# Performance work log

Measured on AMD Instinct MI355X. Metric: run time of the kernel, lower is better.

## Reference

```python
import jax, jax.numpy as jnp
import numpy as np

DECAY = 0.99


def setup_inputs() -> dict:
    key = jax.random.key(0)
    k1, k2, k3, k4 = jax.random.split(key, 4)
    N, D, K = 65536, 256, 1024
    return {
        "masked_z_e_x": jax.random.normal(k1, (N, D), dtype=jnp.float32),
        "z_e_x": jax.random.normal(k2, (N, D), dtype=jnp.float32),
        "embedding": jax.random.normal(k3, (K, D), dtype=jnp.float32) * (1.0 / K),
        "ema_count": jnp.ones((K,), dtype=jnp.float32),
        "ema_w": jax.random.normal(k4, (K, D), dtype=jnp.float32) * (1.0 / K),
    }


def _vq_indices(x_flat, codebook):
    # distances[n,k] = ||x_n||^2 + ||c_k||^2 - 2 x_n . c_k  (addmm in torch)
    c_sqr = jnp.sum(codebook * codebook, axis=1)              # [K]
    x_sqr = jnp.sum(x_flat * x_flat, axis=1, keepdims=True)   # [N,1]
    dists = x_sqr + c_sqr - 2.0 * (x_flat @ codebook.T)       # [N,K]
    return jnp.argmin(dists, axis=1)                          # [N]


def reference(masked_z_e_x, z_e_x, embedding, ema_count, ema_w):
    K, D = embedding.shape
    x_flat = masked_z_e_x.reshape(-1, D)
    indices = _vq_indices(x_flat, embedding)                  # [N] int

    # straight-through quantized codes (value = gathered codes)
    z_q_x = embedding[indices].reshape(masked_z_e_x.shape)

    # EMA codebook update (training branch); one-hot matmul == segment sums
    z_flat = z_e_x.reshape(-1, D)
    counts = jax.ops.segment_sum(jnp.ones_like(indices, dtype=jnp.float32),
                                 indices, num_segments=K)     # [K]
    dw = jax.ops.segment_sum(z_flat, indices, num_segments=K) # [K,D]
    ema_count_new = DECAY * ema_count + (1.0 - DECAY) * counts
    ema_w_new = DECAY * ema_w + (1.0 - DECAY) * dw
    embedding_new = ema_w_new / ema_count_new[:, None]

    # re-gather from the updated (detached) codebook
    z_q_x_bar = embedding_new[indices].reshape(z_e_x.shape)
    return (z_q_x, z_q_x_bar, embedding_new, ema_count_new, ema_w_new)
```

## Files before the change

kernel.cpp:

```cpp
#include <hip/hip_runtime.h>

#define DDIM 256
#define KCODES 1024
#define MARGIN 2.0e-4f

typedef __attribute__((ext_vector_type(8))) short fragA;
typedef __attribute__((ext_vector_type(4))) float f32x4;

static __device__ __forceinline__ float4 ld4(const float* p) {
    return *reinterpret_cast<const float4*>(p);
}

static __device__ __forceinline__ ushort bf16_rne(float f) {
    unsigned bits = __float_as_uint(f);
    unsigned r = bits + 0x7FFFu + ((bits >> 16) & 1u);
    return (ushort)(r >> 16);
}

__global__ void split_sqnorm_kernel(const float* __restrict__ X, ushort* __restrict__ Xs,
                                    float* __restrict__ out, int nrows) {
    int row = blockIdx.x * 4 + (threadIdx.x >> 6);
    if (row >= nrows) return;
    int lane = threadIdx.x & 63;
    float4 v = reinterpret_cast<const float4*>(X + (size_t)row * DDIM)[lane];
    double s = (double)v.x * v.x + (double)v.y * v.y + (double)v.z * v.z + (double)v.w * v.w;
    #pragma unroll
    for (int off = 32; off > 0; off >>= 1) s += __shfl_down(s, off);
    if (lane == 0) out[row] = (float)s;

    float fv[4] = {v.x, v.y, v.z, v.w};
    ushort hb[4], lb[4];
    #pragma unroll
    for (int i = 0; i < 4; i++) {
        hb[i] = bf16_rne(fv[i]);
        float hf = __uint_as_float((unsigned)hb[i] << 16);
        lb[i] = bf16_rne(fv[i] - hf);
    }
    ushort4 hi = make_ushort4(hb[0], hb[1], hb[2], hb[3]);
    ushort4 lo = make_ushort4(lb[0], lb[1], lb[2], lb[3]);
    *reinterpret_cast<ushort4*>(Xs + (size_t)row * 512 + lane * 4) = hi;
    *reinterpret_cast<ushort4*>(Xs + (size_t)row * 512 + 256 + lane * 4) = lo;
}

__global__ __launch_bounds__(256) void argmin_mfma_kernel(
        const float* __restrict__ X, const ushort* __restrict__ Cs,
        float* __restrict__ xsq, const float* __restrict__ csq,
        int* __restrict__ indices, int* __restrict__ flag_cnt,
        int* __restrict__ flag_list, int nrows_total) {
    __shared__ ushort clds[32 * 512];

    int tid = threadIdx.x;
    int w = tid >> 6;
    int l = tid & 63;
    int lm = l & 15;
    int lg = l >> 4;
    int row0 = blockIdx.x * 64;

    const float* xrowf = X + (size_t)(row0 + w * 16 + lm) * DDIM;
    fragA a_hi[8], a_lo[8];
    double dsum = 0.0;
    #pragma unroll
    for (int s = 0; s < 8; s++) {
        float4 v0 = ld4(xrowf + s * 32 + lg * 8);
        float4 v1 = ld4(xrowf + s * 32 + lg * 8 + 4);
        float f[8] = {v0.x, v0.y, v0.z, v0.w, v1.x, v1.y, v1.z, v1.w};
        fragA h, lo;
        #pragma unroll
        for (int j = 0; j < 8; j++) {
            dsum += (double)f[j] * f[j];
            ushort hb = bf16_rne(f[j]);
            float hf = __uint_as_float((unsigned)hb << 16);
            ushort lb = bf16_rne(f[j] - hf);
            h[j] = (short)hb;
            lo[j] = (short)lb;
        }
        a_hi[s] = h;
        a_lo[s] = lo;
    }
    dsum += __shfl_xor(dsum, 16);
    dsum += __shfl_xor(dsum, 32);
    float xsqf = (float)dsum;
    if (l < 16) xsq[row0 + w * 16 + l] = xsqf;
    float xs_r[4];
    #pragma unroll
    for (int r = 0; r < 4; r++) xs_r[r] = __shfl(xsqf, lg * 4 + r);

    float d1[4], d2[4];
    int k1[4];
    #pragma unroll
    for (int r = 0; r < 4; r++) { d1[r] = 3.0e38f; d2[r] = 3.0e38f; k1[r] = 0; }

    for (int kc = 0; kc < KCODES; kc += 32) {
        __syncthreads();
        #pragma unroll
        for (int it = 0; it < 8; it++) {
            int c = it * 256 + tid;
            int r = c >> 6, col = c & 63;
            int p = (col & 32) | ((col & 31) ^ (r & 7));
            *reinterpret_cast<float4*>(&clds[r * 512 + p * 8]) =
                *reinterpret_cast<const float4*>(Cs + (size_t)(kc + r) * 512 + col * 8);
        }
        __syncthreads();

        f32x4 acc[2];
        #pragma unroll
        for (int kt = 0; kt < 2; kt++) acc[kt] = (f32x4){0.f, 0.f, 0.f, 0.f};

        #pragma unroll
        for (int s = 0; s < 8; s++) {
            #pragma unroll
            for (int kt = 0; kt < 2; kt++) {
                int kl = kt * 16 + lm;
                int chi = (4 * s + lg) ^ (kl & 7);
                fragA bhi = *reinterpret_cast<const fragA*>(&clds[kl * 512 + chi * 8]);
                fragA blo = *reinterpret_cast<const fragA*>(&clds[kl * 512 + (32 + chi) * 8]);
                acc[kt] = __builtin_amdgcn_mfma_f32_16x16x32_bf16(a_hi[s], bhi, acc[kt], 0, 0, 0);
                acc[kt] = __builtin_amdgcn_mfma_f32_16x16x32_bf16(a_lo[s], bhi, acc[kt], 0, 0, 0);
                acc[kt] = __builtin_amdgcn_mfma_f32_16x16x32_bf16(a_hi[s], blo, acc[kt], 0, 0, 0);
            }
        }

        #pragma unroll
        for (int kt = 0; kt < 2; kt++) {
            int k = kc + kt * 16 + lm;
            float cs = csq[k];
            #pragma unroll
            for (int r = 0; r < 4; r++) {
                float dist = (xs_r[r] + cs) - 2.0f * acc[kt][r];
                if (dist < d1[r] || (dist == d1[r] && k < k1[r])) {
                    d2[r] = d1[r]; d1[r] = dist; k1[r] = k;
                } else if (dist < d2[r]) {
                    d2[r] = dist;
                }
            }
        }
    }

    #pragma unroll
    for (int r = 0; r < 4; r++) {
        float bd1 = d1[r], bd2 = d2[r];
        int bk1 = k1[r];
        #pragma unroll
        for (int m = 1; m < 16; m <<= 1) {
            float od1 = __shfl_xor(bd1, m);
            int ok1 = __shfl_xor(bk1, m);
            float od2 = __shfl_xor(bd2, m);
            if (od1 < bd1 || (od1 == bd1 && ok1 < bk1)) {
                bd2 = fminf(bd1, od2); bd1 = od1; bk1 = ok1;
            } else {
                bd2 = fminf(bd2, od1);
            }
        }
        if (lm == 0) {
            int row = row0 + w * 16 + lg * 4 + r;
            indices[row] = bk1;
            if (bd2 - bd1 < MARGIN) {
                int pos = atomicAdd(flag_cnt, 1);
                if (pos < nrows_total) flag_list[pos] = row;
            }
        }
    }
}

#define ECH 64
#define NKCH (KCODES / ECH)

__global__ __launch_bounds__(256) void exact_chunk_kernel(
        const float* __restrict__ X, const float* __restrict__ C,
        const float* __restrict__ xsq, const float* __restrict__ csq,
        const int* __restrict__ flag_cnt, const int* __restrict__ flag_list,
        unsigned long long* __restrict__ best64, int nrows_total) {
    __shared__ float xt[64][36];
    __shared__ float ct[64][36];
    __shared__ int rowidx[64];
    __shared__ float xsql[64];

    int cnt = *flag_cnt;
    if (cnt > nrows_total) cnt = nrows_total;
    if (cnt <= 0) return;
    int ntiles = (cnt + 63) >> 6;
    int nunits = ntiles * NKCH;

    int tid = threadIdx.x;
    int tx = tid & 15;
    int ty = tid >> 4;

    for (int u = blockIdx.x; u < nunits; u += gridDim.x) {
        int t = u >> 4;
        int kc = (u & 15) * ECH;
        int base = t * 64;

        __syncthreads();
        if (tid < 64) {
            int p = base + tid;
            int row = flag_list[p < cnt ? p : base];
            rowidx[tid] = row;
            xsql[tid] = xsq[row];
        }
        __syncthreads();

        float xs[4];
        #pragma unroll
        for (int i = 0; i < 4; i++) xs[i] = xsql[i * 16 + ty];

        float acc[4][4];
        #pragma unroll
        for (int i = 0; i < 4; i++)
            #pragma unroll
            for (int j = 0; j < 4; j++) acc[i][j] = 0.0f;

        for (int dt = 0; dt < DDIM; dt += 32) {
            __syncthreads();
            #pragma unroll
            for (int it = 0; it < 2; it++) {
                int e = it * 256 + tid;
                int r = e >> 3, c4 = e & 7;
                *reinterpret_cast<float4*>(&xt[r][c4 * 4]) =
                    ld4(X + (size_t)rowidx[r] * DDIM + dt + c4 * 4);
            }
            #pragma unroll
            for (int it = 0; it < 2; it++) {
                int e = it * 256 + tid;
                int r = e >> 3, c4 = e & 7;
                *reinterpret_cast<float4*>(&ct[r][c4 * 4]) =
                    ld4(C + (size_t)(kc + r) * DDIM + dt + c4 * 4);
            }
            __syncthreads();

            for (int d4 = 0; d4 < 32; d4 += 4) {
                float4 xv[4], cv[4];
                #pragma unroll
                for (int i = 0; i < 4; i++)
                    xv[i] = *reinterpret_cast<const float4*>(&xt[i * 16 + ty][d4]);
                #pragma unroll
                for (int j = 0; j < 4; j++)
                    cv[j] = *reinterpret_cast<const float4*>(&ct[j * 16 + tx][d4]);
                #pragma unroll
                for (int i = 0; i < 4; i++)
                    #pragma unroll
                    for (int j = 0; j < 4; j++) {
                        float a = acc[i][j];
                        a += xv[i].x * cv[j].x; a += xv[i].y * cv[j].y;
                        a += xv[i].z * cv[j].z; a += xv[i].w * cv[j].w;
                        acc[i][j] = a;
                    }
            }
        }

        float cs_r[4];
        #pragma unroll
        for (int j = 0; j < 4; j++) cs_r[j] = csq[kc + j * 16 + tx];

        #pragma unroll
        for (int i = 0; i < 4; i++) {
            float bd = 3.0e38f; int bk = 0;
            #pragma unroll
            for (int j = 0; j < 4; j++) {
                int kk = kc + j * 16 + tx;
                float tt = xs[i] + cs_r[j];
                float dist = tt - 2.0f * acc[i][j];
                if (dist < bd || (dist == bd && kk < bk)) { bd = dist; bk = kk; }
            }
            #pragma unroll
            for (int m = 1; m < 16; m <<= 1) {
                float od = __shfl_xor(bd, m);
                int ok = __shfl_xor(bk, m);
                if (od < bd || (od == bd && ok < bk)) { bd = od; bk = ok; }
            }
            if (tx == 0) {
                int p = base + i * 16 + ty;
                if (p < cnt) {
                    unsigned long long pk =
                        ((unsigned long long)__float_as_uint(bd) << 32) | (unsigned)bk;
                    atomicMin(&best64[p], pk);
                }
            }
        }
    }
}

__global__ void exact_finalize_kernel(const int* __restrict__ flag_cnt,
                                      const int* __restrict__ flag_list,
                                      const unsigned long long* __restrict__ best64,
                                      int* __restrict__ indices, int nrows_total) {
    int cnt = *flag_cnt;
    if (cnt > nrows_total) cnt = nrows_total;
    for (int i = blockIdx.x * 256 + threadIdx.x; i < cnt; i += gridDim.x * 256)
        indices[flag_list[i]] = (int)(best64[i] & 0xFFFFFFFFULL);
}

__global__ void hist_kernel(const int* __restrict__ idx, int* __restrict__ counts) {
    int i = blockIdx.x * 256 + threadIdx.x;
    atomicAdd(&counts[idx[i]], 1);
}

__global__ void prefix_kernel(const int* __restrict__ counts, int* __restrict__ offs,
                              int* __restrict__ cursor) {
    __shared__ int a[KCODES];
    int t = threadIdx.x;
    int v = counts[t];
    a[t] = v;
    __syncthreads();
    for (int s = 1; s < KCODES; s <<= 1) {
        int x = (t >= s) ? a[t - s] : 0;
        __syncthreads();
        a[t] += x;
        __syncthreads();
    }
    int excl = a[t] - v;
    offs[t] = excl;
    cursor[t] = excl;
}

__global__ void scatter_pos_kernel(const int* __restrict__ idx, int* __restrict__ cursor,
                                   int* __restrict__ sorted) {
    int i = blockIdx.x * 256 + threadIdx.x;
    int k = idx[i];
    int pos = atomicAdd(&cursor[k], 1);
    sorted[pos] = i;
}

__global__ __launch_bounds__(256) void segsum_ema_kernel(
        const float* __restrict__ Z, const int* __restrict__ sorted,
        const int* __restrict__ offs, const int* __restrict__ counts,
        const float* __restrict__ ema_count, const float* __restrict__ ema_w,
        float* __restrict__ emb_new, float* __restrict__ cnt_new,
        float* __restrict__ w_new) {
    int k = blockIdx.x;
    int t = threadIdx.x;
    int start = offs[k];
    int cnt = counts[k];

    float acc = 0.f;
    int j = 0;
    for (; j + 4 <= cnt; j += 4) {
        int r0 = sorted[start + j + 0];
        int r1 = sorted[start + j + 1];
        int r2 = sorted[start + j + 2];
        int r3 = sorted[start + j + 3];
        float v0 = Z[(size_t)r0 * DDIM + t];
        float v1 = Z[(size_t)r1 * DDIM + t];
        float v2 = Z[(size_t)r2 * DDIM + t];
        float v3 = Z[(size_t)r3 * DDIM + t];
        acc += v0; acc += v1; acc += v2; acc += v3;
    }
    for (; j < cnt; j++) {
        int r = sorted[start + j];
        acc += Z[(size_t)r * DDIM + t];
    }

    const float DEC = 0.99f;
    const float OMD = (float)(1.0 - 0.99);
    float cn = __fadd_rn(__fmul_rn(DEC, ema_count[k]), __fmul_rn(OMD, (float)cnt));
    float wn = __fadd_rn(__fmul_rn(DEC, ema_w[(size_t)k * DDIM + t]), __fmul_rn(OMD, acc));
    w_new[(size_t)k * DDIM + t] = wn;
    emb_new[(size_t)k * DDIM + t] = __fdiv_rn(wn, cn);
    if (t == 0) cnt_new[k] = cn;
}

__global__ void gather_kernel(const float* __restrict__ emb, const float* __restrict__ emb_new,
                              const int* __restrict__ idx, float* __restrict__ zq,
                              float* __restrict__ zqb) {
    int row = blockIdx.x * 4 + (threadIdx.x >> 6);
    int lane = threadIdx.x & 63;
    int k = idx[row];
    float4 a = reinterpret_cast<const float4*>(emb + (size_t)k * DDIM)[lane];
    float4 b = reinterpret_cast<const float4*>(emb_new + (size_t)k * DDIM)[lane];
    reinterpret_cast<float4*>(zq + (size_t)row * DDIM)[lane] = a;
    reinterpret_cast<float4*>(zqb + (size_t)row * DDIM)[lane] = b;
}

extern "C" void kernel_launch(void* const* d_in, const int* in_sizes, int n_in,
                              void* d_out, int out_size, void* d_ws, size_t ws_size,
                              hipStream_t stream) {
    const float* x = (const float*)d_in[0];
    const float* z = (const float*)d_in[1];
    const float* emb = (const float*)d_in[2];
    const float* ema_count = (const float*)d_in[3];
    const float* ema_w = (const float*)d_in[4];

    const int N = in_sizes[0] / DDIM;
    const int K = in_sizes[3];

    float* out = (float*)d_out;
    float* zq = out;
    float* zqb = zq + (size_t)N * DDIM;
    float* emb_new = zqb + (size_t)N * DDIM;
    float* cnt_new = emb_new + (size_t)K * DDIM;
    float* w_new = cnt_new + K;

    char* wsb = (char*)d_ws;
    size_t off = 0;
    ushort* csplit = (ushort*)(wsb + off); off += (size_t)K * 512 * 2;
    float* xsq = (float*)(wsb + off); off += (size_t)N * 4;
    float* csq = (float*)(wsb + off); off += (size_t)K * 4;
    int* indices = (int*)(wsb + off); off += (size_t)N * 4;
    int* flag_list = (int*)(wsb + off); off += (size_t)N * 4;
    int* sorted = (int*)(wsb + off); off += (size_t)N * 4;
    int* offs = (int*)(wsb + off); off += (size_t)K * 4;
    int* counts = (int*)(wsb + off); off += (size_t)K * 4;
    int* cursor = (int*)(wsb + off); off += (size_t)K * 4;
    int* flag_cnt = (int*)(wsb + off); off += 16;
    unsigned long long* best64 = (unsigned long long*)(wsb + off); off += (size_t)N * 8;

    hipMemsetAsync(counts, 0, (size_t)K * 4 * 2 + 16, stream);
    hipMemsetAsync(best64, 0xFF, (size_t)N * 8, stream);
    split_sqnorm_kernel<<<K / 4, 256, 0, stream>>>(emb, csplit, csq, K);
    argmin_mfma_kernel<<<N / 64, 256, 0, stream>>>(x, csplit, xsq, csq,
                                                   indices, flag_cnt, flag_list, N);
    exact_chunk_kernel<<<256, 256, 0, stream>>>(x, emb, xsq, csq,
                                                flag_cnt, flag_list, best64, N);
    exact_finalize_kernel<<<64, 256, 0, stream>>>(flag_cnt, flag_list, best64, indices, N);
    hist_kernel<<<N / 256, 256, 0, stream>>>(indices, counts);
    prefix_kernel<<<1, KCODES, 0, stream>>>(counts, offs, cursor);
    scatter_pos_kernel<<<N / 256, 256, 0, stream>>>(indices, cursor, sorted);
    segsum_ema_kernel<<<K, 256, 0, stream>>>(z, sorted, offs, counts,
                                             ema_count, ema_w,
                                             emb_new, cnt_new, w_new);
    gather_kernel<<<N / 4, 256, 0, stream>>>(emb, emb_new, indices, zq, zqb);
}
```

Before: 286.7 us.

## Fuse histogram into argmin and gather outputs into segment-sum kernel

Code counts are now accumulated by atomics inside the argmin kernel, and the exact-finalize pass corrects them when a flagged row's index changes. This removes the separate histogram launch. The z_q_x and z_q_x_bar writes move into the per-code segment-sum kernel, which scatters each code's value to the rows listed in sorted order, so the gather kernel and its rereads of the codebook are gone. In exchange, output writes become row-scattered per block, and the load is uneven across codes because of per-code count imbalance.

```diff
diff --git a/kernel.cpp b/kernel.cpp
--- a/kernel.cpp
+++ b/kernel.cpp
@@ -46,7 +46,7 @@
         const float* __restrict__ X, const ushort* __restrict__ Cs,
         float* __restrict__ xsq, const float* __restrict__ csq,
         int* __restrict__ indices, int* __restrict__ flag_cnt,
-        int* __restrict__ flag_list, int nrows_total) {
+        int* __restrict__ flag_list, int* __restrict__ counts, int nrows_total) {
     __shared__ ushort clds[32 * 512];
 
     int tid = threadIdx.x;
@@ -154,6 +154,7 @@
         if (lm == 0) {
             int row = row0 + w * 16 + lg * 4 + r;
             indices[row] = bk1;
+            atomicAdd(&counts[bk1], 1);
             if (bd2 - bd1 < MARGIN) {
                 int pos = atomicAdd(flag_cnt, 1);
                 if (pos < nrows_total) flag_list[pos] = row;
@@ -282,16 +283,20 @@
 __global__ void exact_finalize_kernel(const int* __restrict__ flag_cnt,
                                       const int* __restrict__ flag_list,
                                       const unsigned long long* __restrict__ best64,
-                                      int* __restrict__ indices, int nrows_total) {
+                                      int* __restrict__ indices, int* __restrict__ counts,
+                                      int nrows_total) {
     int cnt = *flag_cnt;
     if (cnt > nrows_total) cnt = nrows_total;
-    for (int i = blockIdx.x * 256 + threadIdx.x; i < cnt; i += gridDim.x * 256)
-        indices[flag_list[i]] = (int)(best64[i] & 0xFFFFFFFFULL);
-}
-
-__global__ void hist_kernel(const int* __restrict__ idx, int* __restrict__ counts) {
-    int i = blockIdx.x * 256 + threadIdx.x;
-    atomicAdd(&counts[idx[i]], 1);
+    for (int i = blockIdx.x * 256 + threadIdx.x; i < cnt; i += gridDim.x * 256) {
+        int row = flag_list[i];
+        int newk = (int)(best64[i] & 0xFFFFFFFFULL);
+        int oldk = indices[row];
+        if (newk != oldk) {
+            indices[row] = newk;
+            atomicAdd(&counts[oldk], -1);
+            atomicAdd(&counts[newk], 1);
+        }
+    }
 }
 
 __global__ void prefix_kernel(const int* __restrict__ counts, int* __restrict__ offs,
@@ -320,12 +325,13 @@
     sorted[pos] = i;
 }
 
-__global__ __launch_bounds__(256) void segsum_ema_kernel(
+__global__ __launch_bounds__(256) void segsum_ema_gather_kernel(
         const float* __restrict__ Z, const int* __restrict__ sorted,
         const int* __restrict__ offs, const int* __restrict__ counts,
         const float* __restrict__ ema_count, const float* __restrict__ ema_w,
+        const float* __restrict__ emb,
         float* __restrict__ emb_new, float* __restrict__ cnt_new,
-        float* __restrict__ w_new) {
+        float* __restrict__ w_new, float* __restrict__ zq, float* __restrict__ zqb) {
     int k = blockIdx.x;
     int t = threadIdx.x;
     int start = offs[k];
@@ -353,21 +359,25 @@
     const float OMD = (float)(1.0 - 0.99);
     float cn = __fadd_rn(__fmul_rn(DEC, ema_count[k]), __fmul_rn(OMD, (float)cnt));
     float wn = __fadd_rn(__fmul_rn(DEC, ema_w[(size_t)k * DDIM + t]), __fmul_rn(OMD, acc));
+    float en = __fdiv_rn(wn, cn);
     w_new[(size_t)k * DDIM + t] = wn;
-    emb_new[(size_t)k * DDIM + t] = __fdiv_rn(wn, cn);
+    emb_new[(size_t)k * DDIM + t] = en;
     if (t == 0) cnt_new[k] = cn;
-}
-
-__global__ void gather_kernel(const float* __restrict__ emb, const float* __restrict__ emb_new,
-                              const int* __restrict__ idx, float* __restrict__ zq,
-                              float* __restrict__ zqb) {
-    int row = blockIdx.x * 4 + (threadIdx.x >> 6);
-    int lane = threadIdx.x & 63;
-    int k = idx[row];
-    float4 a = reinterpret_cast<const float4*>(emb + (size_t)k * DDIM)[lane];
-    float4 b = reinterpret_cast<const float4*>(emb_new + (size_t)k * DDIM)[lane];
-    reinterpret_cast<float4*>(zq + (size_t)row * DDIM)[lane] = a;
-    reinterpret_cast<float4*>(zqb + (size_t)row * DDIM)[lane] = b;
+
+    float embk = emb[(size_t)k * DDIM + t];
+    for (j = 0; j + 2 <= cnt; j += 2) {
+        int r0 = sorted[start + j + 0];
+        int r1 = sorted[start + j + 1];
+        zq[(size_t)r0 * DDIM + t] = embk;
+        zqb[(size_t)r0 * DDIM + t] = en;
+        zq[(size_t)r1 * DDIM + t] = embk;
+        zqb[(size_t)r1 * DDIM + t] = en;
+    }
+    for (; j < cnt; j++) {
+        int r = sorted[start + j];
+        zq[(size_t)r * DDIM + t] = embk;
+        zqb[(size_t)r * DDIM + t] = en;
+    }
 }
 
 extern "C" void kernel_launch(void* const* d_in, const int* in_sizes, int n_in,
@@ -407,15 +417,14 @@
     hipMemsetAsync(best64, 0xFF, (size_t)N * 8, stream);
     split_sqnorm_kernel<<<K / 4, 256, 0, stream>>>(emb, csplit, csq, K);
     argmin_mfma_kernel<<<N / 64, 256, 0, stream>>>(x, csplit, xsq, csq,
-                                                   indices, flag_cnt, flag_list, N);
+                                                   indices, flag_cnt, flag_list, counts, N);
     exact_chunk_kernel<<<256, 256, 0, stream>>>(x, emb, xsq, csq,
                                                 flag_cnt, flag_list, best64, N);
-    exact_finalize_kernel<<<64, 256, 0, stream>>>(flag_cnt, flag_list, best64, indices, N);
-    hist_kernel<<<N / 256, 256, 0, stream>>>(indices, counts);
+    exact_finalize_kernel<<<64, 256, 0, stream>>>(flag_cnt, flag_list, best64,
+                                                  indices, counts, N);
     prefix_kernel<<<1, KCODES, 0, stream>>>(counts, offs, cursor);
     scatter_pos_kernel<<<N / 256, 256, 0, stream>>>(indices, cursor, sorted);
-    segsum_ema_kernel<<<K, 256, 0, stream>>>(z, sorted, offs, counts,
-                                             ema_count, ema_w,
-                                             emb_new, cnt_new, w_new);
-    gather_kernel<<<N / 4, 256, 0, stream>>>(emb, emb_new, indices, zq, zqb);
-}
+    segsum_ema_gather_kernel<<<K, 256, 0, stream>>>(z, sorted, offs, counts,
+                                                    ema_count, ema_w, emb,
+                                                    emb_new, cnt_new, w_new, zq, zqb);
+}
```

Result: faster. 273.2 us (-4.7%).
